# Kernel tuning notes

Hardware: AMD Instinct MI355X
Metric: run time of the kernel (lower is better)

The kernel has to match this reference:

```python
import jax, jax.numpy as jnp
import numpy as np

# dims: batch, fast time, fast/slow embed, heads, rate, ffn hidden, pool hidden, recombine hidden
B, T, D = 2, 2048, 512
H = 8
R = 8
DS = 512
FF = 2048
HP = 2048
HR = 2048


def _ln(x, g, b):
    m = jnp.mean(x, axis=-1, keepdims=True)
    v = jnp.var(x, axis=-1, keepdims=True)
    return (x - m) / jnp.sqrt(v + 1e-5) * g + b


def _encoder_layer(x, ln1_g, ln1_b, wqkv, bqkv, wo, bo, ln2_g, ln2_b, w1, b1, w2, b2, n_heads):
    # pre-LN transformer encoder layer with causal self-attention
    b_, t, d = x.shape
    dh = d // n_heads
    h = _ln(x, ln1_g, ln1_b)
    qkv = h @ wqkv + bqkv  # [B,T,3D]
    q, k, v = jnp.split(qkv, 3, axis=-1)
    q = q.reshape(b_, t, n_heads, dh)
    k = k.reshape(b_, t, n_heads, dh)
    v = v.reshape(b_, t, n_heads, dh)
    scores = jnp.einsum('bqhd,bkhd->bhqk', q, k) / jnp.sqrt(jnp.float32(dh))
    mask = jnp.tril(jnp.ones((t, t), dtype=bool))
    scores = jnp.where(mask, scores, jnp.finfo(scores.dtype).min)
    a = jax.nn.softmax(scores, axis=-1)
    o = jnp.einsum('bhqk,bkhd->bqhd', a, v).reshape(b_, t, d)
    x = x + o @ wo + bo
    h2 = _ln(x, ln2_g, ln2_b)
    return x + jax.nn.gelu(h2 @ w1 + b1) @ w2 + b2


def _pool(f, rate, wp1, bp1, wp2, bp2):
    # causal pooling: s_k = FFN(f_{k*rate : (k+1)*rate}), prepend zero step, drop last
    b_, t, d = f.shape
    k = t // rate
    xb = f[:, :k * rate].reshape(b_, k, rate * d)  # [B,K,rate*D] block flatten
    s = jax.nn.gelu(xb @ wp1 + bp1) @ wp2 + bp2  # [B,K,DS]
    s0 = jnp.zeros((b_, 1, s.shape[-1]), s.dtype)
    return jnp.concatenate([s0, s[:, :-1]], axis=1)


def _recombine(zf, zs, rate, wr1, br1, wr2, br2):
    # lift slow to fast scale (repeat_interleave along time), concat channels, 2-layer MLP
    zl = jnp.repeat(zs, rate, axis=1)[:, :zf.shape[1]]
    x = jnp.concatenate([zf, zl], axis=-1)
    return jax.nn.gelu(x @ wr1 + br1) @ wr2 + br2


def setup_inputs() -> dict:
    key = jax.random.key(0)
    ks = iter(jax.random.split(key, 64))

    def w(shape):
        return jax.random.normal(next(ks), shape, dtype=jnp.float32) * 0.02

    def z(shape):
        return jnp.zeros(shape, dtype=jnp.float32)

    def o(shape):
        return jnp.ones(shape, dtype=jnp.float32)

    inp = {'x': jax.random.normal(next(ks), (B, T, D), dtype=jnp.float32)}
    for suf, dm, ff in (('f', D, FF), ('s', DS, FF)):
        inp['ln1' + suf + '_g'] = o((dm,)); inp['ln1' + suf + '_b'] = z((dm,))
        inp['wqkv_' + suf] = w((dm, 3 * dm)); inp['bqkv_' + suf] = z((3 * dm,))
        inp['wo_' + suf] = w((dm, dm)); inp['bo_' + suf] = z((dm,))
        inp['ln2' + suf + '_g'] = o((dm,)); inp['ln2' + suf + '_b'] = z((dm,))
        inp['w1_' + suf] = w((dm, ff)); inp['b1_' + suf] = z((ff,))
        inp['w2_' + suf] = w((ff, dm)); inp['b2_' + suf] = z((dm,))
    inp['wp1'] = w((R * D, HP)); inp['bp1'] = z((HP,))
    inp['wp2'] = w((HP, DS)); inp['bp2'] = z((DS,))
    inp['wr1'] = w((D + DS, HR)); inp['br1'] = z((HR,))
    inp['wr2'] = w((HR, D)); inp['br2'] = z((D,))
    return inp


def reference(x, ln1f_g, ln1f_b, wqkv_f, bqkv_f, wo_f, bo_f, ln2f_g, ln2f_b, w1_f, b1_f, w2_f, b2_f,
              ln1s_g, ln1s_b, wqkv_s, bqkv_s, wo_s, bo_s, ln2s_g, ln2s_b, w1_s, b1_s, w2_s, b2_s,
              wp1, bp1, wp2, bp2, wr1, br1, wr2, br2):
    # fast-scale encoder layer
    zf = _encoder_layer(x, ln1f_g, ln1f_b, wqkv_f, bqkv_f, wo_f, bo_f,
                        ln2f_g, ln2f_b, w1_f, b1_f, w2_f, b2_f, H)
    # causal pool fast -> slow
    zs_in = _pool(zf, R, wp1, bp1, wp2, bp2)
    # slow-scale encoder layer
    zs = _encoder_layer(zs_in, ln1s_g, ln1s_b, wqkv_s, bqkv_s, wo_s, bo_s,
                        ln2s_g, ln2s_b, w1_s, b1_s, w2_s, b2_s, H)
    # lift + recombine back to fast scale
    return _recombine(zf, zs, R, wr1, br1, wr2, br2)
```

## Files before the change

### kernel.cpp

```cpp
#include <hip/hip_runtime.h>
#include <cstdint>

#define DEV __device__ __forceinline__

typedef float  floatx4 __attribute__((ext_vector_type(4)));
typedef __bf16 bf16x8  __attribute__((ext_vector_type(8)));
typedef short  short8  __attribute__((ext_vector_type(8)));

DEV unsigned short f2bf(float f) {
  unsigned u = __builtin_bit_cast(unsigned, f);
  u += 0x7FFFu + ((u >> 16) & 1u);
  return (unsigned short)(u >> 16);
}
DEV float bf2f(unsigned short s) {
  unsigned u = ((unsigned)s) << 16;
  return __builtin_bit_cast(float, u);
}
DEV float gelu_f(float x) {
  float x3 = x * x * x;
  return 0.5f * x * (1.0f + tanhf(0.7978845608028654f * (x + 0.044715f * x3)));
}

DEV void stage16(const unsigned short* g, unsigned short* l) {
  __builtin_amdgcn_global_load_lds(
      (const __attribute__((address_space(1))) void*)g,
      (__attribute__((address_space(3))) void*)l, 16, 0, 0);
}

struct TrArgs {
  const float* src[12];
  unsigned short* dst[12];
  int K[12];
  int N[12];
  int off[13];
};

__global__ __launch_bounds__(256) void transpose_all_k(TrArgs a) {
  __shared__ unsigned short tile[32][33];
  int bid = blockIdx.x;
  int w = 0;
#pragma unroll
  for (int i = 0; i < 11; ++i) if (bid >= a.off[i + 1]) w = i + 1;
  int loc = bid - a.off[w];
  int tn = a.N[w] >> 5;
  int nt = (loc % tn) * 32, kt = (loc / tn) * 32;
  const float* W = a.src[w];
  unsigned short* WT = a.dst[w];
  int K = a.K[w], N = a.N[w];

  int t = threadIdx.x;
  int rr = t >> 3, c4 = (t & 7) * 4;
  const float* src = W + (size_t)(kt + rr) * N + nt + c4;
  float4 v = *reinterpret_cast<const float4*>(src);
  tile[rr][c4 + 0] = f2bf(v.x); tile[rr][c4 + 1] = f2bf(v.y);
  tile[rr][c4 + 2] = f2bf(v.z); tile[rr][c4 + 3] = f2bf(v.w);
  __syncthreads();
  unsigned short* dst = WT + (size_t)(nt + rr) * K + kt + c4;
  ushort4 o;
  o.x = tile[c4 + 0][rr]; o.y = tile[c4 + 1][rr];
  o.z = tile[c4 + 2][rr]; o.w = tile[c4 + 3][rr];
  *reinterpret_cast<ushort4*>(dst) = o;
}

template <int NP, int ACT, int RES, int OBF>
__global__ __launch_bounds__(256) void reduceN_k(const float* __restrict__ part,
                                                 const float* __restrict__ bias,
                                                 const float* __restrict__ resid,
                                                 void* __restrict__ out,
                                                 int MN, int Nmask) {
  int i = (blockIdx.x * 256 + threadIdx.x) * 4;
  if (i >= MN) return;
  float4 v = *reinterpret_cast<const float4*>(&part[i]);
#pragma unroll
  for (int p = 1; p < NP; ++p) {
    float4 t = *reinterpret_cast<const float4*>(&part[(size_t)p * MN + i]);
    v.x += t.x; v.y += t.y; v.z += t.z; v.w += t.w;
  }
  float4 bv = *reinterpret_cast<const float4*>(&bias[i & Nmask]);
  v.x += bv.x; v.y += bv.y; v.z += bv.z; v.w += bv.w;
  if (RES) {
    float4 r = *reinterpret_cast<const float4*>(&resid[i]);
    v.x += r.x; v.y += r.y; v.z += r.z; v.w += r.w;
  }
  if (ACT) { v.x = gelu_f(v.x); v.y = gelu_f(v.y); v.z = gelu_f(v.z); v.w = gelu_f(v.w); }
  if (OBF) {
    ushort4 o; o.x = f2bf(v.x); o.y = f2bf(v.y); o.z = f2bf(v.z); o.w = f2bf(v.w);
    *reinterpret_cast<ushort4*>(&((unsigned short*)out)[i]) = o;
  } else {
    *reinterpret_cast<float4*>(&((float*)out)[i]) = v;
  }
}

__global__ __launch_bounds__(64) void ln_k(const float* __restrict__ in,
                                           const float* __restrict__ g,
                                           const float* __restrict__ be,
                                           unsigned short* __restrict__ out) {
  int row = blockIdx.x, lane = threadIdx.x;
  const float* p = in + (size_t)row * 512;
  float v[8], s = 0.f, sq = 0.f;
#pragma unroll
  for (int j = 0; j < 8; ++j) { v[j] = p[j * 64 + lane]; s += v[j]; sq += v[j] * v[j]; }
#pragma unroll
  for (int off = 32; off; off >>= 1) { s += __shfl_xor(s, off, 64); sq += __shfl_xor(sq, off, 64); }
  float mean = s * (1.f / 512.f);
  float var  = sq * (1.f / 512.f) - mean * mean;
  float rstd = rsqrtf(var + 1e-5f);
#pragma unroll
  for (int j = 0; j < 8; ++j) {
    int c = j * 64 + lane;
    out[(size_t)row * 512 + c] = f2bf((v[j] - mean) * rstd * g[c] + be[c]);
  }
}

__global__ __launch_bounds__(64) void rsln_k(const float* __restrict__ part,
                                             const float* __restrict__ bias,
                                             const float* __restrict__ g,
                                             const float* __restrict__ be,
                                             float* __restrict__ zsin,
                                             unsigned short* __restrict__ sh) {
  const int MN = 512 * 512;
  int j = blockIdx.x, lane = threadIdx.x;
  int k = j & 255;
  float v[8], s = 0.f, sq = 0.f;
  if (k == 0) {
#pragma unroll
    for (int jj = 0; jj < 8; ++jj) { v[jj] = 0.f; zsin[(size_t)j * 512 + jj * 64 + lane] = 0.f; }
  } else {
    const float* p = part + (size_t)(j - 1) * 512;
#pragma unroll
    for (int jj = 0; jj < 8; ++jj) {
      int c = jj * 64 + lane;
      float t = bias[c];
#pragma unroll
      for (int pp = 0; pp < 4; ++pp) t += p[(size_t)pp * MN + c];
      v[jj] = t;
      zsin[(size_t)j * 512 + c] = t;
      s += t; sq += t * t;
    }
  }
#pragma unroll
  for (int off = 32; off; off >>= 1) { s += __shfl_xor(s, off, 64); sq += __shfl_xor(sq, off, 64); }
  float mean = s * (1.f / 512.f);
  float var  = sq * (1.f / 512.f) - mean * mean;
  float rstd = rsqrtf(var + 1e-5f);
#pragma unroll
  for (int jj = 0; jj < 8; ++jj) {
    int c = jj * 64 + lane;
    sh[(size_t)j * 512 + c] = f2bf((v[jj] - mean) * rstd * g[c] + be[c]);
  }
}

template <int TM, int TN, int ACT, int RES, int OBF, int SPLITK, int CAT = 0>
__global__ __launch_bounds__(256) void gemm_k(const unsigned short* __restrict__ A,
                                              const unsigned short* __restrict__ A2,
                                              const unsigned short* __restrict__ WT,
                                              const float* __restrict__ bias,
                                              const float* __restrict__ resid,
                                              void* __restrict__ out,
                                              int M, int K, int N) {
  constexpr int WMn = (TN == 64) ? 2 : (TM / 64);
  constexpr int WNn = 4 / WMn;
  constexpr int MI  = TM / WMn / 16;
  constexpr int SN  = TN / WNn / 16;
  constexpr int APW = TM / 32;
  constexpr int BPW = TN / 32;
  __shared__ __align__(16) unsigned short As[2][TM * 64];
  __shared__ __align__(16) unsigned short Bs[2][TN * 64];
  const int tid  = threadIdx.x;
  const int wv = tid >> 6, lane = tid & 63;
  const int wm = wv / WNn, wn = wv % WNn;
  const int quad = lane >> 4, l16 = lane & 15;
  const int m0 = blockIdx.y * TM, n0 = blockIdx.x * TN;
  const int sp = (SPLITK > 1) ? blockIdx.z : 0;
  const int Kc = K / SPLITK;
  const int kb0 = sp * Kc;
  const int nk = Kc / 64;
  const int lrow = lane >> 3;
  const int scol = ((lane & 7) ^ lrow) * 8;
  const int sx = l16 & 7;

  floatx4 acc[MI][SN] = {};

  auto stage = [&](int buf, int kb) {
#pragma unroll
    for (int u = 0; u < APW; ++u) {
      int g = wv * APW + u;
      if (CAT) {
        int row = m0 + g * 8 + lrow;
        int kc = kb + scol;
        const unsigned short* s1 = A + (size_t)row * 512 + kc;
        const unsigned short* s2 = A2 +
            ((size_t)((row >> 11) * 256 + ((row & 2047) >> 3))) * 512 + (kc - 512);
        stage16(kc < 512 ? s1 : s2, &As[buf][g * 512]);
      } else {
        stage16(A + (size_t)(m0 + g * 8 + lrow) * K + kb + scol, &As[buf][g * 512]);
      }
    }
#pragma unroll
    for (int u = 0; u < BPW; ++u) {
      int g = wv * BPW + u;
      stage16(WT + (size_t)(n0 + g * 8 + lrow) * K + kb + scol, &Bs[buf][g * 512]);
    }
  };

  stage(0, kb0);
  __syncthreads();

  for (int t = 0; t < nk; ++t) {
    const int buf = t & 1;
    if (t + 1 < nk) stage(buf ^ 1, kb0 + (t + 1) * 64);
    bf16x8 af[MI][2], bfr[SN][2];
#pragma unroll
    for (int i = 0; i < MI; ++i) {
      const int r = wm * (MI * 16) + i * 16 + l16;
#pragma unroll
      for (int kk = 0; kk < 2; ++kk)
        af[i][kk] = *reinterpret_cast<const bf16x8*>(
            &As[buf][r * 64 + (((kk * 4 + quad) ^ sx) * 8)]);
    }
#pragma unroll
    for (int j = 0; j < SN; ++j) {
      const int r = wn * (SN * 16) + j * 16 + l16;
#pragma unroll
      for (int kk = 0; kk < 2; ++kk)
        bfr[j][kk] = *reinterpret_cast<const bf16x8*>(
            &Bs[buf][r * 64 + (((kk * 4 + quad) ^ sx) * 8)]);
    }
#pragma unroll
    for (int i = 0; i < MI; ++i)
#pragma unroll
      for (int j = 0; j < SN; ++j) {
        acc[i][j] = __builtin_amdgcn_mfma_f32_16x16x32_bf16(af[i][0], bfr[j][0], acc[i][j], 0, 0, 0);
        acc[i][j] = __builtin_amdgcn_mfma_f32_16x16x32_bf16(af[i][1], bfr[j][1], acc[i][j], 0, 0, 0);
      }
    __syncthreads();
  }

#pragma unroll
  for (int i = 0; i < MI; ++i) {
    int row_base = m0 + wm * (MI * 16) + i * 16 + quad * 4;
#pragma unroll
    for (int j = 0; j < SN; ++j) {
      int col = n0 + wn * (SN * 16) + j * 16 + l16;
      float bv = (SPLITK > 1) ? 0.f : bias[col];
#pragma unroll
      for (int rr = 0; rr < 4; ++rr) {
        int row = row_base + rr;
        float v = acc[i][j][rr];
        if (SPLITK > 1) {
          ((float*)out)[((size_t)sp * M + row) * N + col] = v;
        } else {
          v += bv;
          if (RES) v += resid[(size_t)row * N + col];
          if (ACT) v = gelu_f(v);
          if (OBF) ((unsigned short*)out)[(size_t)row * N + col] = f2bf(v);
          else     ((float*)out)[(size_t)row * N + col] = v;
        }
      }
    }
  }
}

__global__ __launch_bounds__(256) void attn_k(const unsigned short* __restrict__ qkv,
                                              unsigned short* __restrict__ out, int T) {
  const int ld = 1536, Dm = 512;
  __shared__ unsigned short Ks[2][64 * 72];
  __shared__ unsigned short Vt[2][64 * 72];
  const int tid = threadIdx.x, wv = tid >> 6, lane = tid & 63;
  const int quad = lane >> 4, l16 = lane & 15;
  const int nqt = T >> 6;
  const int z = blockIdx.x;
  const int bh = z & 15;
  const int qt = nqt - 1 - (z >> 4);
  const int b = bh >> 3, hh = bh & 7;
  const int q0 = qt * 64 + wv * 16;
  const size_t bT = (size_t)b * T;

  const unsigned short* qp = qkv + (bT + q0 + l16) * ld + hh * 64 + quad * 8;
  short8 qa = *reinterpret_cast<const short8*>(qp);
  short8 qb = *reinterpret_cast<const short8*>(qp + 32);
  unsigned short qs0[8] __attribute__((aligned(16)));
  unsigned short qs1[8] __attribute__((aligned(16)));
#pragma unroll
  for (int u = 0; u < 8; ++u) {
    qs0[u] = f2bf(bf2f((unsigned short)qa[u]) * 0.125f);
    qs1[u] = f2bf(bf2f((unsigned short)qb[u]) * 0.125f);
  }
  bf16x8 aq0 = *reinterpret_cast<const bf16x8*>(qs0);
  bf16x8 aq1 = *reinterpret_cast<const bf16x8*>(qs1);

  floatx4 O[4] = {};
  float l_sum = 0.f;

  const int nch = qt + 1;
  const int skey = tid >> 2, scc = (tid & 3) * 16;
  const int vkey = (tid & 31) * 2, vdg = tid >> 5;

  short8 kA, kB, vA, vB;
  auto prefetch = [&](int c) {
    const unsigned short* kp = qkv + (bT + c * 64 + skey) * ld + Dm + hh * 64 + scc;
    kA = *reinterpret_cast<const short8*>(kp);
    kB = *reinterpret_cast<const short8*>(kp + 8);
    const unsigned short* vp = qkv + (bT + c * 64 + vkey) * ld + 1024 + hh * 64 + vdg * 8;
    vA = *reinterpret_cast<const short8*>(vp);
    vB = *reinterpret_cast<const short8*>(vp + ld);
  };
  auto stage = [&](int buf) {
    *reinterpret_cast<short8*>(&Ks[buf][skey * 72 + scc])     = kA;
    *reinterpret_cast<short8*>(&Ks[buf][skey * 72 + scc + 8]) = kB;
#pragma unroll
    for (int u = 0; u < 8; ++u) {
      unsigned pk = ((unsigned)(unsigned short)vB[u] << 16) | (unsigned short)vA[u];
      *reinterpret_cast<unsigned*>(&Vt[buf][(vdg * 8 + u) * 72 + vkey]) = pk;
    }
  };

  prefetch(0);
  stage(0);
  __syncthreads();

  for (int c = 0; c < nch; ++c) {
    const int buf = c & 1;
    const bool last = (c == nch - 1);
    if (!last) prefetch(c + 1);

    floatx4 S[4];
    __builtin_amdgcn_s_setprio(1);
#pragma unroll
    for (int sub = 0; sub < 4; ++sub) {
      const unsigned short* kr = &Ks[buf][(sub * 16 + l16) * 72 + quad * 8];
      bf16x8 k0 = *reinterpret_cast<const bf16x8*>(kr);
      bf16x8 k1 = *reinterpret_cast<const bf16x8*>(kr + 32);
      floatx4 sacc = {};
      sacc = __builtin_amdgcn_mfma_f32_16x16x32_bf16(k0, aq0, sacc, 0, 0, 0);
      sacc = __builtin_amdgcn_mfma_f32_16x16x32_bf16(k1, aq1, sacc, 0, 0, 0);
      S[sub] = sacc;
    }
    __builtin_amdgcn_s_setprio(0);

    if (last) {
      const int k0g = c * 64;
      const int qg = q0 + l16;
#pragma unroll
      for (int sub = 0; sub < 4; ++sub)
#pragma unroll
        for (int r = 0; r < 4; ++r) {
          int kg = k0g + sub * 16 + quad * 4 + r;
          if (kg > qg) S[sub][r] = -3.0e38f;
        }
    }
#pragma unroll
    for (int sub = 0; sub < 4; ++sub)
#pragma unroll
      for (int r = 0; r < 4; ++r) {
        float p = __expf(S[sub][r]);
        S[sub][r] = p;
        l_sum += p;
      }

    short8 p0, p1;
#pragma unroll
    for (int j = 0; j < 4; ++j) {
      p0[j]     = (short)f2bf(S[0][j]);
      p0[4 + j] = (short)f2bf(S[1][j]);
      p1[j]     = (short)f2bf(S[2][j]);
      p1[4 + j] = (short)f2bf(S[3][j]);
    }
    bf16x8 pa0 = __builtin_bit_cast(bf16x8, p0);
    bf16x8 pa1 = __builtin_bit_cast(bf16x8, p1);

    __builtin_amdgcn_s_setprio(1);
#pragma unroll
    for (int sd = 0; sd < 4; ++sd) {
      const unsigned short* vr = &Vt[buf][(sd * 16 + l16) * 72 + quad * 4];
      short4 v0a = *reinterpret_cast<const short4*>(vr);
      short4 v0b = *reinterpret_cast<const short4*>(vr + 16);
      short4 v1a = *reinterpret_cast<const short4*>(vr + 32);
      short4 v1b = *reinterpret_cast<const short4*>(vr + 48);
      short8 w0, w1;
      w0[0]=v0a.x; w0[1]=v0a.y; w0[2]=v0a.z; w0[3]=v0a.w;
      w0[4]=v0b.x; w0[5]=v0b.y; w0[6]=v0b.z; w0[7]=v0b.w;
      w1[0]=v1a.x; w1[1]=v1a.y; w1[2]=v1a.z; w1[3]=v1a.w;
      w1[4]=v1b.x; w1[5]=v1b.y; w1[6]=v1b.z; w1[7]=v1b.w;
      O[sd] = __builtin_amdgcn_mfma_f32_16x16x32_bf16(pa0, __builtin_bit_cast(bf16x8, w0), O[sd], 0, 0, 0);
      O[sd] = __builtin_amdgcn_mfma_f32_16x16x32_bf16(pa1, __builtin_bit_cast(bf16x8, w1), O[sd], 0, 0, 0);
    }
    __builtin_amdgcn_s_setprio(0);

    if (!last) stage((c + 1) & 1);
    __syncthreads();
  }

  l_sum += __shfl_xor(l_sum, 16, 64);
  l_sum += __shfl_xor(l_sum, 32, 64);
  float lq[4];
#pragma unroll
  for (int r = 0; r < 4; ++r)
    lq[r] = __shfl(l_sum, quad * 4 + r, 64);

#pragma unroll
  for (int sd = 0; sd < 4; ++sd)
#pragma unroll
    for (int r = 0; r < 4; ++r) {
      int qg = q0 + quad * 4 + r;
      out[(bT + qg) * Dm + hh * 64 + sd * 16 + l16] = f2bf(O[sd][r] / lq[r]);
    }
}

extern "C" void kernel_launch(void* const* d_in, const int* in_sizes, int n_in,
                              void* d_out, int out_size, void* d_ws, size_t ws_size,
                              hipStream_t stream) {
  (void)in_sizes; (void)n_in; (void)out_size; (void)ws_size;
  const int B = 2, T = 2048, FF = 2048, HP = 2048, HR = 2048;
  const int BT = B * T;
  const int BK = B * 256;

  const float* x      = (const float*)d_in[0];
  const float* ln1f_g = (const float*)d_in[1];
  const float* ln1f_b = (const float*)d_in[2];
  const float* wqkv_f = (const float*)d_in[3];
  const float* bqkv_f = (const float*)d_in[4];
  const float* wo_f   = (const float*)d_in[5];
  const float* bo_f   = (const float*)d_in[6];
  const float* ln2f_g = (const float*)d_in[7];
  const float* ln2f_b = (const float*)d_in[8];
  const float* w1_f   = (const float*)d_in[9];
  const float* b1_f   = (const float*)d_in[10];
  const float* w2_f   = (const float*)d_in[11];
  const float* b2_f   = (const float*)d_in[12];
  const float* ln1s_g = (const float*)d_in[13];
  const float* ln1s_b = (const float*)d_in[14];
  const float* wqkv_s = (const float*)d_in[15];
  const float* bqkv_s = (const float*)d_in[16];
  const float* wo_s   = (const float*)d_in[17];
  const float* bo_s   = (const float*)d_in[18];
  const float* ln2s_g = (const float*)d_in[19];
  const float* ln2s_b = (const float*)d_in[20];
  const float* w1_s   = (const float*)d_in[21];
  const float* b1_s   = (const float*)d_in[22];
  const float* w2_s   = (const float*)d_in[23];
  const float* b2_s   = (const float*)d_in[24];
  const float* wp1    = (const float*)d_in[25];
  const float* bp1    = (const float*)d_in[26];
  const float* wp2    = (const float*)d_in[27];
  const float* bp2    = (const float*)d_in[28];
  const float* wr1    = (const float*)d_in[29];
  const float* br1    = (const float*)d_in[30];
  const float* wr2    = (const float*)d_in[31];
  const float* br2    = (const float*)d_in[32];

  char* ws = (char*)d_ws;
  const size_t HMB = 512 * 1024;
  unsigned short* wtbase = (unsigned short*)(ws);
  unsigned short* h      = (unsigned short*)(ws + 76  * HMB);
  unsigned short* qkv    = (unsigned short*)(ws + 84  * HMB);
  unsigned short* attn   = (unsigned short*)(ws + 108 * HMB);
  float*          x1     = (float*)(ws + 116 * HMB);
  unsigned short* mid    = (unsigned short*)(ws + 132 * HMB);
  unsigned short* zf     = (unsigned short*)(ws + 164 * HMB);
  unsigned short* pmid   = (unsigned short*)(ws + 84  * HMB);
  float*          zsin   = (float*)(ws + 90  * HMB);
  unsigned short* sh     = (unsigned short*)(ws + 92  * HMB);
  unsigned short* sqkv   = (unsigned short*)(ws + 93  * HMB);
  unsigned short* sattn  = (unsigned short*)(ws + 96  * HMB);
  float*          sx1    = (float*)(ws + 97  * HMB);
  unsigned short* smid   = (unsigned short*)(ws + 99  * HMB);
  unsigned short* szs    = (unsigned short*)(ws + 103 * HMB);
  float*          part   = (float*)(ws + 172 * HMB);
  unsigned short* mid2   = (unsigned short*)(ws + 240 * HMB);

  size_t wo_off = 0;
  auto walloc = [&](size_t n) { unsigned short* p = wtbase + wo_off; wo_off += n; return p; };
  unsigned short* t_qkv_f = walloc((size_t)512 * 1536);
  unsigned short* t_wo_f  = walloc((size_t)512 * 512);
  unsigned short* t_w1_f  = walloc((size_t)512 * 2048);
  unsigned short* t_w2_f  = walloc((size_t)2048 * 512);
  unsigned short* t_qkv_s = walloc((size_t)512 * 1536);
  unsigned short* t_wo_s  = walloc((size_t)512 * 512);
  unsigned short* t_w1_s  = walloc((size_t)512 * 2048);
  unsigned short* t_w2_s  = walloc((size_t)2048 * 512);
  unsigned short* t_wp1   = walloc((size_t)4096 * 2048);
  unsigned short* t_wp2   = walloc((size_t)2048 * 512);
  unsigned short* t_wr1   = walloc((size_t)1024 * 2048);
  unsigned short* t_wr2   = walloc((size_t)2048 * 512);

  {
    TrArgs a;
    const float* srcs[12] = {wqkv_f, wo_f, w1_f, w2_f, wqkv_s, wo_s, w1_s, w2_s,
                             wp1, wp2, wr1, wr2};
    unsigned short* dsts[12] = {t_qkv_f, t_wo_f, t_w1_f, t_w2_f, t_qkv_s, t_wo_s,
                                t_w1_s, t_w2_s, t_wp1, t_wp2, t_wr1, t_wr2};
    int Ks[12] = {512, 512, 512, 2048, 512, 512, 512, 2048, 4096, 2048, 1024, 2048};
    int Ns[12] = {1536, 512, 2048, 512, 1536, 512, 2048, 512, 2048, 512, 2048, 512};
    int off = 0;
    for (int i = 0; i < 12; ++i) {
      a.src[i] = srcs[i]; a.dst[i] = dsts[i]; a.K[i] = Ks[i]; a.N[i] = Ns[i];
      a.off[i] = off;
      off += (Ks[i] / 32) * (Ns[i] / 32);
    }
    a.off[12] = off;
    transpose_all_k<<<off, 256, 0, stream>>>(a);
  }

  ln_k<<<BT, 64, 0, stream>>>(x, ln1f_g, ln1f_b, h);
  gemm_k<64, 128, 0, 0, 1, 1><<<dim3(12, 64), 256, 0, stream>>>(h, nullptr, t_qkv_f, bqkv_f, nullptr, qkv, BT, 512, 1536);
  attn_k<<<(T / 64) * 16, 256, 0, stream>>>(qkv, attn, T);
  gemm_k<64, 64, 0, 1, 0, 1><<<dim3(8, 64), 256, 0, stream>>>(attn, nullptr, t_wo_f, bo_f, x, x1, BT, 512, 512);
  ln_k<<<BT, 64, 0, stream>>>(x1, ln2f_g, ln2f_b, h);
  gemm_k<128, 128, 1, 0, 1, 1><<<dim3(16, 32), 256, 0, stream>>>(h, nullptr, t_w1_f, b1_f, nullptr, mid, BT, 512, FF);
  gemm_k<64, 64, 0, 1, 1, 1><<<dim3(8, 64), 256, 0, stream>>>(mid, nullptr, t_w2_f, b2_f, x1, zf, BT, FF, 512);

  gemm_k<128, 128, 0, 0, 0, 4><<<dim3(16, 4, 4), 256, 0, stream>>>(zf, nullptr, t_wp1, nullptr, nullptr, part, BK, 4096, HP);
  reduceN_k<4, 1, 0, 1><<<(BK * HP) / 1024, 256, 0, stream>>>(part, bp1, nullptr, pmid, BK * HP, HP - 1);
  gemm_k<64, 64, 0, 0, 0, 4><<<dim3(8, 8, 4), 256, 0, stream>>>(pmid, nullptr, t_wp2, nullptr, nullptr, part, BK, HP, 512);
  rsln_k<<<BK, 64, 0, stream>>>(part, bp2, ln1s_g, ln1s_b, zsin, sh);

  gemm_k<64, 64, 0, 0, 1, 1><<<dim3(24, 8), 256, 0, stream>>>(sh, nullptr, t_qkv_s, bqkv_s, nullptr, sqkv, BK, 512, 1536);
  attn_k<<<(256 / 64) * 16, 256, 0, stream>>>(sqkv, sattn, 256);
  gemm_k<64, 64, 0, 1, 0, 1><<<dim3(8, 8), 256, 0, stream>>>(sattn, nullptr, t_wo_s, bo_s, zsin, sx1, BK, 512, 512);
  ln_k<<<BK, 64, 0, stream>>>(sx1, ln2s_g, ln2s_b, sh);
  gemm_k<64, 64, 1, 0, 1, 1><<<dim3(32, 8), 256, 0, stream>>>(sh, nullptr, t_w1_s, b1_s, nullptr, smid, BK, 512, FF);
  gemm_k<64, 64, 0, 1, 1, 1><<<dim3(8, 8), 256, 0, stream>>>(smid, nullptr, t_w2_s, b2_s, sx1, szs, BK, FF, 512);

  gemm_k<128, 128, 1, 0, 1, 1, 1><<<dim3(16, 32), 256, 0, stream>>>(zf, szs, t_wr1, br1, nullptr, mid2, BT, 1024, HR);
  gemm_k<64, 64, 0, 0, 0, 1><<<dim3(8, 64), 256, 0, stream>>>(mid2, nullptr, t_wr2, br2, nullptr, d_out, BT, HR, 512);
}
```

Before: 430.8 us.

## Split causal attention key range into segments with separate reduction kernel

```diff
diff --git a/kernel.cpp b/kernel.cpp
--- a/kernel.cpp
+++ b/kernel.cpp
@@ -262,16 +262,22 @@
 }
 
 __global__ __launch_bounds__(256) void attn_k(const unsigned short* __restrict__ qkv,
-                                              unsigned short* __restrict__ out, int T) {
+                                              unsigned short* __restrict__ out,
+                                              float* __restrict__ pO,
+                                              float* __restrict__ pl, int T) {
   const int ld = 1536, Dm = 512;
   __shared__ unsigned short Ks[2][64 * 72];
   __shared__ unsigned short Vt[2][64 * 72];
   const int tid = threadIdx.x, wv = tid >> 6, lane = tid & 63;
   const int quad = lane >> 4, l16 = lane & 15;
-  const int nqt = T >> 6;
-  const int z = blockIdx.x;
-  const int bh = z & 15;
-  const int qt = nqt - 1 - (z >> 4);
+  const int bh = blockIdx.x;
+  const int qt = blockIdx.y;
+  const int seg = blockIdx.z;
+  const int nch = qt + 1;
+  const int nseg = (nch + 7) >> 3;
+  if (seg >= nseg) return;
+  const int c0 = seg * 8;
+  const int c1 = min(c0 + 8, nch);
   const int b = bh >> 3, hh = bh & 7;
   const int q0 = qt * 64 + wv * 16;
   const size_t bT = (size_t)b * T;
@@ -292,7 +298,6 @@
   floatx4 O[4] = {};
   float l_sum = 0.f;
 
-  const int nch = qt + 1;
   const int skey = tid >> 2, scc = (tid & 3) * 16;
   const int vkey = (tid & 31) * 2, vdg = tid >> 5;
 
@@ -315,14 +320,14 @@
     }
   };
 
-  prefetch(0);
+  prefetch(c0);
   stage(0);
   __syncthreads();
 
-  for (int c = 0; c < nch; ++c) {
-    const int buf = c & 1;
-    const bool last = (c == nch - 1);
-    if (!last) prefetch(c + 1);
+  for (int c = c0; c < c1; ++c) {
+    const int buf = (c - c0) & 1;
+    const bool segEnd = (c == c1 - 1);
+    if (!segEnd) prefetch(c + 1);
 
     floatx4 S[4];
     __builtin_amdgcn_s_setprio(1);
@@ -338,7 +343,7 @@
     }
     __builtin_amdgcn_s_setprio(0);
 
-    if (last) {
+    if (c == nch - 1) {
       const int k0g = c * 64;
       const int qg = q0 + l16;
 #pragma unroll
@@ -387,24 +392,67 @@
     }
     __builtin_amdgcn_s_setprio(0);
 
-    if (!last) stage((c + 1) & 1);
+    if (!segEnd) stage((c - c0 + 1) & 1);
     __syncthreads();
   }
 
   l_sum += __shfl_xor(l_sum, 16, 64);
   l_sum += __shfl_xor(l_sum, 32, 64);
-  float lq[4];
-#pragma unroll
-  for (int r = 0; r < 4; ++r)
-    lq[r] = __shfl(l_sum, quad * 4 + r, 64);
-
-#pragma unroll
-  for (int sd = 0; sd < 4; ++sd)
-#pragma unroll
-    for (int r = 0; r < 4; ++r) {
-      int qg = q0 + quad * 4 + r;
-      out[(bT + qg) * Dm + hh * 64 + sd * 16 + l16] = f2bf(O[sd][r] / lq[r]);
-    }
+
+  if (nseg == 1) {
+    float lq[4];
+#pragma unroll
+    for (int r = 0; r < 4; ++r)
+      lq[r] = __shfl(l_sum, quad * 4 + r, 64);
+#pragma unroll
+    for (int sd = 0; sd < 4; ++sd)
+#pragma unroll
+      for (int r = 0; r < 4; ++r) {
+        int qg = q0 + quad * 4 + r;
+        out[(bT + qg) * Dm + hh * 64 + sd * 16 + l16] = f2bf(O[sd][r] / lq[r]);
+      }
+  } else {
+    const int tile = (bh * 32 + qt) * 4 + seg;
+    float* po = pO + (size_t)tile * 4096;
+#pragma unroll
+    for (int sd = 0; sd < 4; ++sd)
+#pragma unroll
+      for (int r = 0; r < 4; ++r)
+        po[(wv * 16 + quad * 4 + r) * 64 + sd * 16 + l16] = O[sd][r];
+    if (quad == 0) pl[(size_t)tile * 64 + wv * 16 + l16] = l_sum;
+  }
+}
+
+__global__ __launch_bounds__(256) void attnred_k(const float* __restrict__ pO,
+                                                 const float* __restrict__ pl,
+                                                 unsigned short* __restrict__ out, int T) {
+  const int bh = blockIdx.x, qt = blockIdx.y + 8;
+  const int nseg = (qt >> 3) + 1;
+  const int b = bh >> 3, hh = bh & 7;
+  const int t = threadIdx.x;
+  const int q = t >> 2, dg = (t & 3) * 16;
+  const int tbase = (bh * 32 + qt) * 4;
+  float l = 0.f;
+  for (int s = 0; s < nseg; ++s) l += pl[(size_t)(tbase + s) * 64 + q];
+  float acc[16] = {};
+  for (int s = 0; s < nseg; ++s) {
+    const float* p = pO + (size_t)(tbase + s) * 4096 + q * 64 + dg;
+#pragma unroll
+    for (int j = 0; j < 4; ++j) {
+      float4 v = *reinterpret_cast<const float4*>(&p[j * 4]);
+      acc[j * 4 + 0] += v.x; acc[j * 4 + 1] += v.y;
+      acc[j * 4 + 2] += v.z; acc[j * 4 + 3] += v.w;
+    }
+  }
+  float inv = 1.f / l;
+  unsigned short* o = out + ((size_t)b * T + qt * 64 + q) * 512 + hh * 64 + dg;
+#pragma unroll
+  for (int j = 0; j < 4; ++j) {
+    ushort4 w;
+    w.x = f2bf(acc[j * 4 + 0] * inv); w.y = f2bf(acc[j * 4 + 1] * inv);
+    w.z = f2bf(acc[j * 4 + 2] * inv); w.w = f2bf(acc[j * 4 + 3] * inv);
+    *reinterpret_cast<ushort4*>(&o[j * 4]) = w;
+  }
 }
 
 extern "C" void kernel_launch(void* const* d_in, const int* in_sizes, int n_in,
@@ -467,6 +515,7 @@
   unsigned short* smid   = (unsigned short*)(ws + 99  * HMB);
   unsigned short* szs    = (unsigned short*)(ws + 103 * HMB);
   float*          part   = (float*)(ws + 172 * HMB);
+  float*          pl     = (float*)(ws + 236 * HMB);
   unsigned short* mid2   = (unsigned short*)(ws + 240 * HMB);
 
   size_t wo_off = 0;
@@ -504,7 +553,8 @@
 
   ln_k<<<BT, 64, 0, stream>>>(x, ln1f_g, ln1f_b, h);
   gemm_k<64, 128, 0, 0, 1, 1><<<dim3(12, 64), 256, 0, stream>>>(h, nullptr, t_qkv_f, bqkv_f, nullptr, qkv, BT, 512, 1536);
-  attn_k<<<(T / 64) * 16, 256, 0, stream>>>(qkv, attn, T);
+  attn_k<<<dim3(16, T / 64, 4), 256, 0, stream>>>(qkv, attn, part, pl, T);
+  attnred_k<<<dim3(16, T / 64 - 8), 256, 0, stream>>>(part, pl, attn, T);
   gemm_k<64, 64, 0, 1, 0, 1><<<dim3(8, 64), 256, 0, stream>>>(attn, nullptr, t_wo_f, bo_f, x, x1, BT, 512, 512);
   ln_k<<<BT, 64, 0, stream>>>(x1, ln2f_g, ln2f_b, h);
   gemm_k<128, 128, 1, 0, 1, 1><<<dim3(16, 32), 256, 0, stream>>>(h, nullptr, t_w1_f, b1_f, nullptr, mid, BT, 512, FF);
@@ -516,7 +566,7 @@
   rsln_k<<<BK, 64, 0, stream>>>(part, bp2, ln1s_g, ln1s_b, zsin, sh);
 
   gemm_k<64, 64, 0, 0, 1, 1><<<dim3(24, 8), 256, 0, stream>>>(sh, nullptr, t_qkv_s, bqkv_s, nullptr, sqkv, BK, 512, 1536);
-  attn_k<<<(256 / 64) * 16, 256, 0, stream>>>(sqkv, sattn, 256);
+  attn_k<<<dim3(16, 4, 1), 256, 0, stream>>>(sqkv, sattn, part, pl, 256);
   gemm_k<64, 64, 0, 1, 0, 1><<<dim3(8, 8), 256, 0, stream>>>(sattn, nullptr, t_wo_s, bo_s, zsin, sx1, BK, 512, 512);
   ln_k<<<BK, 64, 0, stream>>>(sx1, ln2s_g, ln2s_b, sh);
   gemm_k<64, 64, 1, 0, 1, 1><<<dim3(32, 8), 256, 0, stream>>>(sh, nullptr, t_w1_s, b1_s, nullptr, smid, BK, 512, FF);
```

Result: slower. 535.6 us (+24.3%).
